# Optimization experiments

Measured on AMD Instinct MI355X. Metric: run time of the kernel, lower is better.

The kernel has to match this reference:

```python
import jax, jax.numpy as jnp
import numpy as np

WINDOW = 1
BETA = 0.01
EPS = 1e-6


def conv3x3(x, W, b):
    y = jax.lax.conv_general_dilated(x, W, (1, 1), 'SAME',
                                     dimension_numbers=('NCHW', 'OIHW', 'NCHW'))
    return y + b[None, :, None, None]


def grid_sample_bilinear(feat, gx, gy):
    # feat [n,C,H,W]; gx,gy [n,h,w] normalized to [-1,1]; align_corners=True, zeros padding
    n, C, H, W = feat.shape
    ix = (gx + 1.0) * 0.5 * (W - 1)
    iy = (gy + 1.0) * 0.5 * (H - 1)
    x0 = jnp.floor(ix)
    y0 = jnp.floor(iy)
    wx = ix - x0
    wy = iy - y0

    def corner(xc, yc, wgt):
        valid = (xc >= 0) & (xc <= W - 1) & (yc >= 0) & (yc <= H - 1)
        xi = jnp.clip(xc, 0, W - 1).astype(jnp.int32)
        yi = jnp.clip(yc, 0, H - 1).astype(jnp.int32)
        g = jax.vmap(lambda f, yy, xx: f[:, yy, xx])(feat, yi, xi)  # [n,C,h,w]
        return g * (wgt * valid)[:, None, :, :]

    return (corner(x0, y0, (1 - wx) * (1 - wy)) +
            corner(x0 + 1, y0, wx * (1 - wy)) +
            corner(x0, y0 + 1, (1 - wx) * wy) +
            corner(x0 + 1, y0 + 1, wx * wy))


def random_pooling(gt, rand, h, w):
    # adaptive_max_pool2d with exact-division output -> uniform block max pool
    n, c, H, W = gt.shape
    kh, kw = H // h, W // w
    rm = rand * (gt > 0.1)
    blocks = rm.reshape(n, c, h, kh, w, kw).transpose(0, 1, 2, 4, 3, 5)
    blocks = blocks.reshape(n, c, h, w, kh * kw)
    loc = jnp.argmax(blocks, axis=-1)
    bi, bj = loc // kw, loc % kw
    row = jnp.arange(h, dtype=jnp.int32)[:, None] * kh + bi
    col = jnp.arange(w, dtype=jnp.int32)[None, :] * kw + bj
    indices = row * W + col  # flat indices into H*W, [n,c,h,w]
    gtf = gt.reshape(n, c, H * W)
    rg = jnp.take_along_axis(gtf, indices.reshape(n, c, h * w), axis=-1)
    rg = rg.reshape(n, c, h, w)
    rg = jnp.where(rg < 0.1, 0.0, rg)
    return rg, indices


def log_grads(rg, window):
    # windowed log-gradients in 4 directions per offset distance
    n, c, h, w = rg.shape
    image = jnp.pad(rg, ((0, 0), (0, 0), (window, window), (window, window)))
    limg = jnp.log(image + EPS)
    mask = image > 0.1
    lc = limg[:, :, window:window + h, window:window + w]
    mc = mask[:, :, window:window + h, window:window + w]
    gs, ms = [], []
    for dd in range(1, window + 1):
        for ox, oy in ((0, dd), (dd, dd), (dd, 0), (dd, -dd)):
            sx, sy = window + ox, window + oy
            gs.append(lc - limg[:, :, sx:sx + h, sy:sy + w])
            ms.append(mc & mask[:, :, sx:sx + h, sy:sy + w])
    return jnp.concatenate(gs, 1), jnp.concatenate(ms, 1)


def single_loss(rand_i, x, d, gts, W_att, b_att, W_post, b_post):
    n, c, h, w = d.shape
    H, W = gts.shape[2], gts.shape[3]
    rg, indices = random_pooling(gts, rand_i, h, w)
    bias = W // w // 2 + (H // h // 2) * W
    indices = indices + bias
    ind_x = 2.0 * ((indices % W).astype(d.dtype) / W - 0.5)
    ind_y = 2.0 * ((indices // W).astype(d.dtype) / H - 0.5)
    feat = grid_sample_bilinear(x, ind_x[:, 0], ind_y[:, 0])
    att = jax.nn.sigmoid(conv3x3(feat, W_att, b_att))
    ds = conv3x3(att * d, W_post, b_post)
    grad_gt, grad_mk = log_grads(rg, WINDOW)
    a = jnp.abs(ds - grad_gt)
    sl1 = jnp.where(a < BETA, 0.5 * a * a / BETA, a - 0.5 * BETA)
    mk = grad_mk.astype(ds.dtype)
    return (sl1 * mk).sum() / mk.sum()


def setup_inputs() -> dict:
    key = jax.random.key(0)
    ks = jax.random.split(key, 8)
    n, H, W = 4, 480, 640
    h, w = 120, 160
    DC, FC, R = 32, 32, 20  # r = 5 * 4 * window
    return {
        'x': jax.random.normal(ks[0], (n, FC, H, W), dtype=jnp.float32),
        'd': jax.random.normal(ks[1], (n, DC, h, w), dtype=jnp.float32),
        'gts': jax.random.uniform(ks[2], (n, 1, H, W), dtype=jnp.float32),
        'rand': jax.random.uniform(ks[3], (R, n, 1, H, W), dtype=jnp.float32),
        'W_att': jax.random.normal(ks[4], (DC, FC, 3, 3), dtype=jnp.float32) * 0.05,
        'b_att': jnp.zeros((DC,), dtype=jnp.float32),
        'W_post': jax.random.normal(ks[5], (4 * WINDOW, DC, 3, 3), dtype=jnp.float32) * 0.05,
        'b_post': jnp.zeros((4 * WINDOW,), dtype=jnp.float32),
    }


def reference(x, d, gts, rand, W_att, b_att, W_post, b_post):
    def step(acc, r_i):
        return acc + single_loss(r_i, x, d, gts, W_att, b_att, W_post, b_post), None
    total, _ = jax.lax.scan(step, jnp.float32(0.0), rand)
    return total / rand.shape[0]
```

## Files before the change

### kernel.cpp

```cpp
#include <hip/hip_runtime.h>
#include <math.h>

#define NN 4
#define FC 32
#define DC 32
#define HH 480
#define WW 640
#define hh 120
#define ww 160
#define RR 20
#define TILE 14
#define ATT 16
#define FT 18
#define BIAS_IDX 1282
#define CP 16
#define LOGEPS -13.815511f
#define MTHR   -8.0f

#define WS_W1T 64
#define WS_W2T 9280
#define WS_WB1 10432
#define WS_WB2 15040
#define WS_RED 19648
#define WS_RG  20480
#define WS_IDX 1556480
#define WS_XB  3092480
#define XB_COUNT ((size_t)NN * HH * WW * 16)
#define WS_NEED_BYTES (((size_t)WS_XB + XB_COUNT) * 4)

#define XPACK_B0 1
#define XPACK_NB (HH * NN)
#define POOL_B0  (XPACK_B0 + XPACK_NB)
#define POOL_CB  (hh * ww / 256)
#define POOL_NB  (POOL_CB * NN * RR)
#define SETUP_NB (POOL_B0 + POOL_NB)

typedef __attribute__((ext_vector_type(8))) short short8;
typedef __attribute__((ext_vector_type(4))) float f32x4;
typedef __attribute__((ext_vector_type(2))) float f32x2;

__device__ __forceinline__ unsigned int bf16pack(float a, float b) {
    unsigned int ua = __float_as_uint(a);
    ua = (ua + 0x7fffu + ((ua >> 16) & 1u)) >> 16;
    unsigned int ub = __float_as_uint(b);
    ub = (ub + 0x7fffu + ((ub >> 16) & 1u)) >> 16;
    return ua | (ub << 16);
}
__device__ __forceinline__ unsigned short bf16r(float f) {
    unsigned int u = __float_as_uint(f);
    u = (u + 0x7fffu + ((u >> 16) & 1u)) >> 16;
    return (unsigned short)u;
}
__device__ __forceinline__ float bf16tof(unsigned short s) {
    return __uint_as_float(((unsigned int)s) << 16);
}

__global__ void setup_kernel(const float* __restrict__ x, const float* __restrict__ gts,
                             const float* __restrict__ rnd,
                             const float* __restrict__ W_att, const float* __restrict__ W_post,
                             float* __restrict__ ws) {
    const int b = blockIdx.x;
    const int tid = threadIdx.x;

    if (b == 0) {
        if (tid < 2*RR) ws[tid] = 0.f;
        for (int i = tid; i < RR*16*2; i += 256) ws[WS_RED + i] = 0.f;
        float* w1t = ws + WS_W1T;
        float* w2t = ws + WS_W2T;
        for (int i = tid; i < 32*32*9; i += 256) {
            int oc = i / (32*9); int rem = i % (32*9); int c = rem / 9; int tap = rem % 9;
            w1t[(tap*32 + c)*32 + oc] = W_att[i];
        }
        for (int i = tid; i < 4*32*9; i += 256) {
            int oc = i / (32*9); int rem = i % (32*9); int c = rem / 9; int tap = rem % 9;
            w2t[(tap*32 + c)*4 + oc] = W_post[i];
        }
        unsigned int* wb = (unsigned int*)(ws + WS_WB1);
        for (int i = tid; i < 9*2*64; i += 256) {
            int lane = i & 63; int th = i >> 6;
            int t = th >> 1, h2 = th & 1;
            int q = lane >> 4, col = lane & 15, oc = h2*16 + col;
            unsigned int vv[4];
            #pragma unroll
            for (int j = 0; j < 4; ++j) {
                int c0 = 8*q + 2*j;
                float f0 = W_att[(oc*32 + c0    )*9 + t];
                float f1 = W_att[(oc*32 + c0 + 1)*9 + t];
                vv[j] = bf16pack(f0, f1);
            }
            uint4 v4; v4.x = vv[0]; v4.y = vv[1]; v4.z = vv[2]; v4.w = vv[3];
            ((uint4*)wb)[i] = v4;
        }
        unsigned int* wb2 = (unsigned int*)(ws + WS_WB2);
        for (int i = tid; i < 9*2*64; i += 256) {
            int lane = i & 63; int th = i >> 6;
            int t = th >> 1, part = th & 1;
            int q = lane >> 4, oc = lane & 15;
            unsigned int vv[4];
            #pragma unroll
            for (int j = 0; j < 4; ++j) {
                int c0 = 8*q + 2*j;
                float f0 = (oc < 4) ? W_post[(oc*32 + c0    )*9 + t] : 0.f;
                float f1 = (oc < 4) ? W_post[(oc*32 + c0 + 1)*9 + t] : 0.f;
                if (part == 0) {
                    vv[j] = ((unsigned int)bf16r(f0)) | (((unsigned int)bf16r(f1)) << 16);
                } else {
                    float l0 = f0 - bf16tof(bf16r(f0));
                    float l1 = f1 - bf16tof(bf16r(f1));
                    vv[j] = ((unsigned int)bf16r(l0)) | (((unsigned int)bf16r(l1)) << 16);
                }
            }
            uint4 v4; v4.x = vv[0]; v4.y = vv[1]; v4.z = vv[2]; v4.w = vv[3];
            ((uint4*)wb2)[i] = v4;
        }
    } else if (b < POOL_B0) {
        const int bb = b - XPACK_B0;
        const int y = bb % HH;
        const int n = bb / HH;
        unsigned int* xb = (unsigned int*)(ws + WS_XB);
        for (int px = tid; px < WW; px += 256) {
            unsigned int* o = xb + ((size_t)(n*HH + y)*WW + px) * 16;
            uint4 v[4];
            #pragma unroll
            for (int k = 0; k < 4; ++k) {
                #pragma unroll
                for (int j = 0; j < 4; ++j) {
                    int cp = 4*k + j;
                    float f0 = x[((size_t)(n*FC + 2*cp    )*HH + y)*WW + px];
                    float f1 = x[((size_t)(n*FC + 2*cp + 1)*HH + y)*WW + px];
                    ((unsigned int*)&v[k])[j] = bf16pack(f0, f1);
                }
            }
            #pragma unroll
            for (int k = 0; k < 4; ++k) ((uint4*)o)[k] = v[k];
        }
    } else {
        const int bb = b - POOL_B0;
        const int r  = bb / (POOL_CB * NN);
        const int rem = bb % (POOL_CB * NN);
        const int n  = rem / POOL_CB;
        const int cb = rem % POOL_CB;
        const int cell = cb * 256 + tid;
        const int h = cell / ww, w = cell % ww;
        const float* gt_n = gts + (size_t)n * HH * WW;
        const float* rd_n = rnd + ((size_t)r * NN + n) * (size_t)(HH * WW);
        float best = -1.f, bg = 0.f; int bii = 0, bjj = 0;
        #pragma unroll
        for (int bi = 0; bi < 4; ++bi) {
            const float4 g4 = *(const float4*)(gt_n + (size_t)(h*4 + bi)*WW + w*4);
            const float4 r4 = *(const float4*)(rd_n + (size_t)(h*4 + bi)*WW + w*4);
            const float gv[4] = {g4.x, g4.y, g4.z, g4.w};
            const float rv[4] = {r4.x, r4.y, r4.z, r4.w};
            #pragma unroll
            for (int bj = 0; bj < 4; ++bj) {
                float rm = (gv[bj] > 0.1f) ? rv[bj] : 0.f;
                if (rm > best) { best = rm; bii = bi; bjj = bj; bg = gv[bj]; }
            }
        }
        int idx_b = (h*4 + bii) * WW + (w*4 + bjj) + BIAS_IDX;
        size_t o = ((size_t)(r*NN + n) * (hh*ww)) + cell;
        float g2 = (bg < 0.1f) ? 0.f : bg;
        ((float*)(ws + WS_RG))[o] = logf(g2 + 1e-6f);
        ((unsigned int*)(ws + WS_IDX))[o] = ((unsigned int)(idx_b / WW) << 16) | (unsigned int)(idx_b % WW);
    }
}

__launch_bounds__(256, 4)
__global__ void wvl_main(const unsigned int* __restrict__ xb, const float* __restrict__ d,
                         const float* __restrict__ b_att, const float* __restrict__ b_post,
                         float* __restrict__ ws) {
    __shared__ unsigned int s_feat[FT * FT * 16];
    __shared__ float s_plog[FT * FT];
    __shared__ float s_rn[4], s_rd[4];

    const float* lg_all  = (const float*)(ws + WS_RG);
    const unsigned int* pidx_all = (const unsigned int*)(ws + WS_IDX);

    const int tid = threadIdx.x;

    const int f   = blockIdx.x;
    const int xcd = f & 7;
    const int bb  = f >> 3;
    const int gi  = bb / 120;
    const int ii  = bb % 120;
    const int band = gi * 8 + xcd;
    const int n   = band / 18;
    const int rem = band % 18;
    const int ty  = rem >> 1;
    const int tx  = (rem & 1) * 6 + (ii % 6);
    const int r   = ii / 6;

    const int py0 = ty * TILE - 2;
    const int px0 = tx * TILE - 2;

    const size_t pbase = (size_t)(r*NN + n) * (hh*ww);

    for (int p = tid; p < FT * FT; p += 256) {
        int pi = p / FT, pj = p % FT;
        int gi2 = py0 + pi, gj = px0 + pj;
        float lval = LOGEPS;
        if (gi2 >= 0 && gi2 < hh && gj >= 0 && gj < ww)
            lval = lg_all[pbase + (size_t)gi2 * ww + gj];
        s_plog[p] = lval;
    }

    for (int p = tid; p < FT * FT; p += 256) {
        int pi = p / FT, pj = p % FT;
        int gi2 = py0 + pi, gj = px0 + pj;
        unsigned int* dst = &s_feat[p * 16];
        const int sw = (p >> 1) & 3;
        if (gi2 < 0 || gi2 >= hh || gj < 0 || gj >= ww) {
            uint4 z; z.x = z.y = z.z = z.w = 0u;
            #pragma unroll
            for (int k = 0; k < 4; ++k) ((uint4*)dst)[k] = z;
            continue;
        }
        unsigned int pk = pidx_all[pbase + (size_t)gi2 * ww + gj];
        int rr2 = (int)(pk >> 16);
        int cc  = (int)(pk & 0xffff);
        float gxf = 2.0f * ((float)cc  / (float)WW - 0.5f);
        float gyf = 2.0f * ((float)rr2 / (float)HH - 0.5f);
        float ix = (gxf + 1.0f) * 0.5f * (float)(WW - 1);
        float iy = (gyf + 1.0f) * 0.5f * (float)(HH - 1);
        float x0f = floorf(ix), y0f = floorf(iy);
        float wx = ix - x0f, wy = iy - y0f;
        int x0 = (int)x0f, y0 = (int)y0f;
        float vx0 = (x0f >= 0.f        && x0f <= (float)(WW-1)) ? 1.f : 0.f;
        float vx1 = (x0f + 1.f >= 0.f  && x0f + 1.f <= (float)(WW-1)) ? 1.f : 0.f;
        float vy0 = (y0f >= 0.f        && y0f <= (float)(HH-1)) ? 1.f : 0.f;
        float vy1 = (y0f + 1.f >= 0.f  && y0f + 1.f <= (float)(HH-1)) ? 1.f : 0.f;
        int xi0 = min(max(x0, 0), WW-1),  xi1 = min(max(x0+1, 0), WW-1);
        int yi0 = min(max(y0, 0), HH-1),  yi1 = min(max(y0+1, 0), HH-1);
        float w00 = (1.f-wx)*(1.f-wy) * (vx0*vy0);
        float w10 = wx*(1.f-wy)       * (vx1*vy0);
        float w01 = (1.f-wx)*wy       * (vx0*vy1);
        float w11 = wx*wy             * (vx1*vy1);
        const f32x2 vw00 = {w00, w00}, vw10 = {w10, w10}, vw01 = {w01, w01}, vw11 = {w11, w11};
        const uint4* q00 = (const uint4*)(xb + ((size_t)(n*HH + yi0)*WW + xi0) * 16);
        const uint4* q10 = (const uint4*)(xb + ((size_t)(n*HH + yi0)*WW + xi1) * 16);
        const uint4* q01 = (const uint4*)(xb + ((size_t)(n*HH + yi1)*WW + xi0) * 16);
        const uint4* q11 = (const uint4*)(xb + ((size_t)(n*HH + yi1)*WW + xi1) * 16);
        #pragma unroll
        for (int k = 0; k < 4; ++k) {
            uint4 A = q00[k], B = q10[k], C = q01[k], D = q11[k];
            uint4 o;
            #pragma unroll
            for (int j = 0; j < 4; ++j) {
                unsigned int ua = ((const unsigned int*)&A)[j];
                unsigned int ub = ((const unsigned int*)&B)[j];
                unsigned int uc = ((const unsigned int*)&C)[j];
                unsigned int ud = ((const unsigned int*)&D)[j];
                f32x2 va = {__uint_as_float(ua << 16), __uint_as_float(ua & 0xffff0000u)};
                f32x2 vb = {__uint_as_float(ub << 16), __uint_as_float(ub & 0xffff0000u)};
                f32x2 vc = {__uint_as_float(uc << 16), __uint_as_float(uc & 0xffff0000u)};
                f32x2 vd = {__uint_as_float(ud << 16), __uint_as_float(ud & 0xffff0000u)};
                f32x2 acc = vw00 * va;
                acc += vw10 * vb;
                acc += vw01 * vc;
                acc += vw11 * vd;
                ((unsigned int*)&o)[j] = bf16pack(acc.x, acc.y);
            }
            ((uint4*)dst)[k ^ sw] = o;
        }
    }
    __syncthreads();

    const int lane = tid & 63;
    const int wv   = tid >> 6;
    const int mcol = lane & 15;
    const int q    = lane >> 4;

    f32x4 acc1[4][2];
    {
        float bb0 = b_att[mcol];
        float bb1 = b_att[mcol + 16];
        #pragma unroll
        for (int rr = 0; rr < 4; ++rr) {
            acc1[rr][0] = (f32x4){bb0, bb0, bb0, bb0};
            acc1[rr][1] = (f32x4){bb1, bb1, bb1, bb1};
        }
    }
    {
        const uint4* wB = (const uint4*)(ws + WS_WB1);
        #pragma unroll
        for (int t = 0; t < 9; ++t) {
            union { uint4 u; short8 s; } b0u, b1u;
            b0u.u = wB[(t*2 + 0)*64 + lane];
            b1u.u = wB[(t*2 + 1)*64 + lane];
            const int dy = t / 3, dx = t % 3;
            #pragma unroll
            for (int rr = 0; rr < 4; ++rr) {
                int ay = wv*4 + rr;
                int pix = (ay + dy) * FT + dx + mcol;
                union { uint4 u; short8 s; } a;
                a.u = *(const uint4*)&s_feat[pix * 16 + (q ^ ((pix >> 1) & 3)) * 4];
                acc1[rr][0] = __builtin_amdgcn_mfma_f32_16x16x32_bf16(a.s, b0u.s, acc1[rr][0], 0, 0, 0);
                acc1[rr][1] = __builtin_amdgcn_mfma_f32_16x16x32_bf16(a.s, b1u.s, acc1[rr][1], 0, 0, 0);
            }
        }
    }
    __syncthreads();

    {
        unsigned short* attd16 = (unsigned short*)s_feat;
        #pragma unroll
        for (int rr = 0; rr < 4; ++rr) {
            int ay = wv*4 + rr;
            int gy = ty * TILE - 1 + ay;
            bool gyok = (gy >= 0 && gy < hh);
            #pragma unroll
            for (int h2 = 0; h2 < 2; ++h2) {
                int oc = mcol + 16*h2;
                const float* drow = d + ((size_t)(n*DC + oc) * hh + (gyok ? gy : 0)) * ww;
                #pragma unroll
                for (int reg = 0; reg < 4; ++reg) {
                    int ax = 4*q + reg;
                    int gx = tx * TILE - 1 + ax;
                    float av = __builtin_amdgcn_rcpf(1.f + __expf(-acc1[rr][h2][reg]));
                    float dv = (gyok && gx >= 0 && gx < ww) ? drow[gx] : 0.f;
                    int pix = ay * ATT + ax;
                    int dwi = pix * 16 + ((oc >> 3) ^ ((pix >> 1) & 3)) * 4 + ((oc >> 1) & 3);
                    attd16[dwi * 2 + (oc & 1)] = bf16r(av * dv);
                }
            }
        }
    }
    __syncthreads();

    float num_t = 0.f, den_t = 0.f;
    {
        const uint4* wB2 = (const uint4*)(ws + WS_WB2);
        const int qy0 = wv * 4;
        float bias2 = (mcol < 4) ? b_post[mcol] : 0.f;
        f32x4 acc2[4];
        #pragma unroll
        for (int rr = 0; rr < 4; ++rr) acc2[rr] = (f32x4){bias2, bias2, bias2, bias2};
        #pragma unroll
        for (int t = 0; t < 9; ++t) {
            union { uint4 u; short8 s; } bh, bl;
            bh.u = wB2[(t*2 + 0)*64 + lane];
            bl.u = wB2[(t*2 + 1)*64 + lane];
            const int dy = t / 3, dx = t % 3;
            #pragma unroll
            for (int rr = 0; rr < 4; ++rr) {
                if (qy0 + rr >= TILE) break;
                int pix = (qy0 + rr + dy) * ATT + (mcol + dx);
                union { uint4 u; short8 s; } a;
                a.u = *(const uint4*)&s_feat[pix * 16 + (q ^ ((pix >> 1) & 3)) * 4];
                acc2[rr] = __builtin_amdgcn_mfma_f32_16x16x32_bf16(a.s, bh.s, acc2[rr], 0, 0, 0);
                acc2[rr] = __builtin_amdgcn_mfma_f32_16x16x32_bf16(a.s, bl.s, acc2[rr], 0, 0, 0);
            }
        }
        const int o3 = mcol & 3;
        const int oy = (o3 == 0) ? 0 : 1;
        const int ox = (o3 == 3) ? -1 : ((o3 == 2) ? 0 : 1);
        #pragma unroll
        for (int rr = 0; rr < 4; ++rr) {
            if (qy0 + rr >= TILE) break;
            int qy = qy0 + rr;
            int gy2 = ty * TILE + qy;
            bool rowok = (gy2 < hh);
            #pragma unroll
            for (int reg = 0; reg < 4; ++reg) {
                int qx = 4*q + reg;
                int gx2 = tx * TILE + qx;
                float lc = s_plog[(qy + 2) * FT + (qx + 2)];
                float ln = s_plog[(qy + 2 + oy) * FT + (qx + 2 + ox)];
                bool m = rowok && (qx < TILE) && (gx2 < ww) && (mcol < 4)
                       && (lc > MTHR) && (ln > MTHR);
                float a2 = fabsf(acc2[rr][reg] - (lc - ln));
                float sl1 = (a2 < 0.01f) ? (50.f * a2 * a2) : (a2 - 0.005f);
                if (m) { num_t += sl1; den_t += 1.f; }
            }
        }
    }

    for (int off = 32; off > 0; off >>= 1) {
        num_t += __shfl_down(num_t, off);
        den_t += __shfl_down(den_t, off);
    }
    if (lane == 0) { s_rn[wv] = num_t; s_rd[wv] = den_t; }
    __syncthreads();
    if (tid == 0) {
        int slot = r * 16 + (bb & 15);
        atomicAdd(&ws[WS_RED + slot*2],     s_rn[0] + s_rn[1] + s_rn[2] + s_rn[3]);
        atomicAdd(&ws[WS_RED + slot*2 + 1], s_rd[0] + s_rd[1] + s_rd[2] + s_rd[3]);
    }
}

__launch_bounds__(256, 6)
__global__ void wvl_fallback(const float* __restrict__ x, const float* __restrict__ d,
                             const float* __restrict__ gts, const float* __restrict__ rnd,
                             const float* __restrict__ b_att, const float* __restrict__ b_post,
                             float* __restrict__ ws) {
    __shared__ unsigned int s_buf[CP * FT * FT];
    __shared__ float s_pgt[FT * FT];
    __shared__ int   s_pidx[FT * FT];
    __shared__ float s_rn[4], s_rd[4];

    const float* w1t = ws + WS_W1T;
    const float* w2t = ws + WS_W2T;

    const int tid = threadIdx.x;
    const int tilesx = (ww + TILE - 1) / TILE;
    const int tx = blockIdx.x % tilesx;
    const int ty = blockIdx.x / tilesx;
    const int n  = blockIdx.y;
    const int r  = blockIdx.z;
    const int py0 = ty * TILE - 2;
    const int px0 = tx * TILE - 2;

    const float* gt_n = gts + (size_t)n * HH * WW;
    const float* rd_n = rnd + ((size_t)r * NN + n) * (size_t)(HH * WW);
    for (int p = tid; p < FT * FT; p += 256) {
        int pi = p / FT, pj = p % FT;
        int gi = py0 + pi, gj = px0 + pj;
        float gval = 0.f; int idx = -1;
        if (gi >= 0 && gi < hh && gj >= 0 && gj < ww) {
            float best = -1.f; int bii = 0, bjj = 0; float bg = 0.f;
            #pragma unroll
            for (int bi = 0; bi < 4; ++bi) {
                const float* gr = gt_n + (size_t)(gi*4 + bi) * WW + gj*4;
                const float* rp = rd_n + (size_t)(gi*4 + bi) * WW + gj*4;
                #pragma unroll
                for (int bj = 0; bj < 4; ++bj) {
                    float g  = gr[bj];
                    float rv = rp[bj];
                    float rm = (g > 0.1f) ? rv : 0.f;
                    if (rm > best) { best = rm; bii = bi; bjj = bj; bg = g; }
                }
            }
            gval = bg;
            idx = (gi*4 + bii) * WW + (gj*4 + bjj) + BIAS_IDX;
        }
        s_pgt[p]  = gval;
        s_pidx[p] = idx;
    }
    __syncthreads();

    const float* x_n = x + (size_t)n * FC * HH * WW;
    for (int p = tid; p < FT * FT; p += 256) {
        int idx = s_pidx[p];
        if (idx < 0) {
            #pragma unroll
            for (int cp = 0; cp < CP; ++cp) s_buf[cp * (FT*FT) + p] = 0u;
            continue;
        }
        int cc = idx % WW;
        int rr2 = idx / WW;
        float gxf = 2.0f * ((float)cc  / (float)WW - 0.5f);
        float gyf = 2.0f * ((float)rr2 / (float)HH - 0.5f);
        float ix = (gxf + 1.0f) * 0.5f * (float)(WW - 1);
        float iy = (gyf + 1.0f) * 0.5f * (float)(HH - 1);
        float x0f = floorf(ix), y0f = floorf(iy);
        float wx = ix - x0f, wy = iy - y0f;
        int x0 = (int)x0f, y0 = (int)y0f;
        float vx0 = (x0f >= 0.f        && x0f <= (float)(WW-1)) ? 1.f : 0.f;
        float vx1 = (x0f + 1.f >= 0.f  && x0f + 1.f <= (float)(WW-1)) ? 1.f : 0.f;
        float vy0 = (y0f >= 0.f        && y0f <= (float)(HH-1)) ? 1.f : 0.f;
        float vy1 = (y0f + 1.f >= 0.f  && y0f + 1.f <= (float)(HH-1)) ? 1.f : 0.f;
        int xi0 = min(max(x0, 0), WW-1),  xi1 = min(max(x0+1, 0), WW-1);
        int yi0 = min(max(y0, 0), HH-1),  yi1 = min(max(y0+1, 0), HH-1);
        float w00 = (1.f-wx)*(1.f-wy) * (vx0*vy0);
        float w10 = wx*(1.f-wy)       * (vx1*vy0);
        float w01 = (1.f-wx)*wy       * (vx0*vy1);
        float w11 = wx*wy             * (vx1*vy1);
        const float* p00 = x_n + (size_t)yi0 * WW + xi0;
        const float* p10 = x_n + (size_t)yi0 * WW + xi1;
        const float* p01 = x_n + (size_t)yi1 * WW + xi0;
        const float* p11 = x_n + (size_t)yi1 * WW + xi1;
        #pragma unroll 4
        for (int cp = 0; cp < CP; ++cp) {
            int o0 = (2*cp)     * (HH * WW);
            int o1 = (2*cp + 1) * (HH * WW);
            float f0 = w00 * p00[o0] + w10 * p10[o0] + w01 * p01[o0] + w11 * p11[o0];
            float f1 = w00 * p00[o1] + w10 * p10[o1] + w01 * p01[o1] + w11 * p11[o1];
            s_buf[cp * (FT*FT) + p] = bf16pack(f0, f1);
        }
    }
    __syncthreads();

    const int ay = tid >> 4, ax = tid & 15;
    float acc[32];
    #pragma unroll
    for (int oc = 0; oc < 32; ++oc) acc[oc] = b_att[oc];
    for (int dy = 0; dy < 3; ++dy) {
        for (int dx = 0; dx < 3; ++dx) {
            const float* wt = w1t + (dy*3 + dx) * 1024;
            int base = (ay + dy) * FT + (ax + dx);
            for (int cp = 0; cp < CP; ++cp) {
                unsigned int u = s_buf[cp * (FT*FT) + base];
                float f0 = __uint_as_float(u << 16);
                float f1 = __uint_as_float(u & 0xffff0000u);
                const float* wp0 = wt + (2*cp) * 32;
                const float* wp1 = wp0 + 32;
                #pragma unroll
                for (int oc = 0; oc < 32; ++oc) acc[oc] = fmaf(f0, wp0[oc], acc[oc]);
                #pragma unroll
                for (int oc = 0; oc < 32; ++oc) acc[oc] = fmaf(f1, wp1[oc], acc[oc]);
            }
        }
    }
    __syncthreads();
    {
        int gy = ty * TILE - 1 + ay;
        int gx = tx * TILE - 1 + ax;
        bool inb = (gy >= 0 && gy < hh && gx >= 0 && gx < ww);
        const float* d_n = d + (size_t)n * DC * hh * ww;
        #pragma unroll
        for (int cp = 0; cp < CP; ++cp) {
            float a0 = 1.f / (1.f + __expf(-acc[2*cp]));
            float a1 = 1.f / (1.f + __expf(-acc[2*cp+1]));
            float v0 = 0.f, v1 = 0.f;
            if (inb) {
                v0 = a0 * d_n[(size_t)((2*cp)   * hh + gy) * ww + gx];
                v1 = a1 * d_n[(size_t)((2*cp+1) * hh + gy) * ww + gx];
            }
            s_buf[cp * (ATT*ATT) + tid] = bf16pack(v0, v1);
        }
    }
    __syncthreads();

    float num_t = 0.f, den_t = 0.f;
    if (tid < TILE * TILE) {
        int qy = tid / TILE, qx = tid % TILE;
        int gy2 = ty * TILE + qy, gx2 = tx * TILE + qx;
        if (gy2 < hh && gx2 < ww) {
            float acc2[4];
            #pragma unroll
            for (int k = 0; k < 4; ++k) acc2[k] = b_post[k];
            for (int dy = 0; dy < 3; ++dy) {
                for (int dx = 0; dx < 3; ++dx) {
                    const float* wt = w2t + (dy*3 + dx) * 128;
                    int base = (qy + dy) * ATT + (qx + dx);
                    for (int cp = 0; cp < CP; ++cp) {
                        unsigned int u = s_buf[cp * (ATT*ATT) + base];
                        float f0 = __uint_as_float(u << 16);
                        float f1 = __uint_as_float(u & 0xffff0000u);
                        const float* wp0 = wt + (2*cp) * 4;
                        const float* wp1 = wp0 + 4;
                        #pragma unroll
                        for (int k2 = 0; k2 < 4; ++k2) acc2[k2] = fmaf(f0, wp0[k2], acc2[k2]);
                        #pragma unroll
                        for (int k2 = 0; k2 < 4; ++k2) acc2[k2] = fmaf(f1, wp1[k2], acc2[k2]);
                    }
                }
            }
            int pc = (qy + 2) * FT + (qx + 2);
            float rgc = s_pgt[pc]; rgc = (rgc < 0.1f) ? 0.f : rgc;
            float lc = logf(rgc + 1e-6f);
            bool  mc = rgc > 0.1f;
            const int oys[4] = {0, 1, 1, 1};
            const int oxs[4] = {1, 1, 0, -1};
            #pragma unroll
            for (int k = 0; k < 4; ++k) {
                int pnb = (qy + 2 + oys[k]) * FT + (qx + 2 + oxs[k]);
                float rgn = s_pgt[pnb]; rgn = (rgn < 0.1f) ? 0.f : rgn;
                float ln = logf(rgn + 1e-6f);
                bool m = mc && (rgn > 0.1f);
                float gg = lc - ln;
                float a2 = fabsf(acc2[k] - gg);
                float sl1 = (a2 < 0.01f) ? (0.5f * a2 * a2 / 0.01f) : (a2 - 0.005f);
                if (m) { num_t += sl1; den_t += 1.f; }
            }
        }
    }
    for (int off = 32; off > 0; off >>= 1) {
        num_t += __shfl_down(num_t, off);
        den_t += __shfl_down(den_t, off);
    }
    int wid = tid >> 6, lane = tid & 63;
    if (lane == 0) { s_rn[wid] = num_t; s_rd[wid] = den_t; }
    __syncthreads();
    if (tid == 0) {
        int slot = r * 16 + (blockIdx.x & 15);
        atomicAdd(&ws[WS_RED + slot*2],     s_rn[0] + s_rn[1] + s_rn[2] + s_rn[3]);
        atomicAdd(&ws[WS_RED + slot*2 + 1], s_rd[0] + s_rd[1] + s_rd[2] + s_rd[3]);
    }
}

__global__ void finish_kernel(const float* __restrict__ ws, float* __restrict__ out) {
    __shared__ float sn[RR], sd[RR];
    const int tid = threadIdx.x;
    if (tid < RR) { sn[tid] = 0.f; sd[tid] = 0.f; }
    __syncthreads();
    if (tid < RR * 16) {
        int r2 = tid >> 4;
        atomicAdd(&sn[r2], ws[WS_RED + tid*2]);
        atomicAdd(&sd[r2], ws[WS_RED + tid*2 + 1]);
    }
    __syncthreads();
    if (tid == 0) {
        float s = 0.f;
        for (int r2 = 0; r2 < RR; ++r2) s += sn[r2] / sd[r2];
        out[0] = s / (float)RR;
    }
}

extern "C" void kernel_launch(void* const* d_in, const int* in_sizes, int n_in,
                              void* d_out, int out_size, void* d_ws, size_t ws_size,
                              hipStream_t stream) {
    const float* x      = (const float*)d_in[0];
    const float* d      = (const float*)d_in[1];
    const float* gts    = (const float*)d_in[2];
    const float* rnd    = (const float*)d_in[3];
    const float* W_att  = (const float*)d_in[4];
    const float* b_att  = (const float*)d_in[5];
    const float* W_post = (const float*)d_in[6];
    const float* b_post = (const float*)d_in[7];
    float* out = (float*)d_out;
    float* ws  = (float*)d_ws;

    const int tilesx = (ww + TILE - 1) / TILE;
    const int tilesy = (hh + TILE - 1) / TILE;

    if (ws_size >= WS_NEED_BYTES) {
        hipLaunchKernelGGL(setup_kernel, dim3(SETUP_NB), dim3(256), 0, stream,
                           x, gts, rnd, W_att, W_post, ws);
        unsigned int* xb = (unsigned int*)(ws + WS_XB);
        hipLaunchKernelGGL(wvl_main, dim3(tilesx * tilesy * NN * RR), dim3(256), 0, stream,
                           xb, d, b_att, b_post, ws);
    } else {
        hipLaunchKernelGGL(setup_kernel, dim3(1), dim3(256), 0, stream,
                           x, gts, rnd, W_att, W_post, ws);
        dim3 grid2(tilesx * tilesy, NN, RR);
        hipLaunchKernelGGL(wvl_fallback, grid2, dim3(256), 0, stream,
                           x, d, gts, rnd, b_att, b_post, ws);
    }

    hipLaunchKernelGGL(finish_kernel, dim3(1), dim3(512), 0, stream, ws, out);
}
```

Before: 581.0 us.

## Pre-pack d channel-last and transpose MFMA operands for vectorized epilogues

Adds a setup stage that repacks the depth feature tensor d into a per-pixel channel-contiguous layout in the workspace. Swaps the A/B operands of both MFMA convolutions so each lane holds four consecutive output channels of one pixel. The attention-times-d epilogue can then use two float4 loads and two packed 8-byte LDS stores, replacing many scattered scalar global loads and 2-byte shared stores. The loss epilogue now reads one centre log value per row. This costs an extra workspace buffer and an extra pass over d in setup, which is repeated work across the 20 random draws only once.

```diff
diff --git a/kernel.cpp b/kernel.cpp
--- a/kernel.cpp
+++ b/kernel.cpp
@@ -26,14 +26,18 @@
 #define WS_IDX 1556480
 #define WS_XB  3092480
 #define XB_COUNT ((size_t)NN * HH * WW * 16)
-#define WS_NEED_BYTES (((size_t)WS_XB + XB_COUNT) * 4)
+#define WS_DPK (WS_XB + 19660800)
+#define DPK_COUNT ((size_t)NN * hh * ww * 32)
+#define WS_NEED_BYTES (((size_t)WS_DPK + DPK_COUNT) * 4)
 
 #define XPACK_B0 1
 #define XPACK_NB (HH * NN)
 #define POOL_B0  (XPACK_B0 + XPACK_NB)
 #define POOL_CB  (hh * ww / 256)
 #define POOL_NB  (POOL_CB * NN * RR)
-#define SETUP_NB (POOL_B0 + POOL_NB)
+#define DPK_B0   (POOL_B0 + POOL_NB)
+#define DPK_NB   (NN * hh)
+#define SETUP_NB (DPK_B0 + DPK_NB)
 
 typedef __attribute__((ext_vector_type(8))) short short8;
 typedef __attribute__((ext_vector_type(4))) float f32x4;
@@ -55,8 +59,8 @@
     return __uint_as_float(((unsigned int)s) << 16);
 }
 
-__global__ void setup_kernel(const float* __restrict__ x, const float* __restrict__ gts,
-                             const float* __restrict__ rnd,
+__global__ void setup_kernel(const float* __restrict__ x, const float* __restrict__ d,
+                             const float* __restrict__ gts, const float* __restrict__ rnd,
                              const float* __restrict__ W_att, const float* __restrict__ W_post,
                              float* __restrict__ ws) {
     const int b = blockIdx.x;
@@ -134,7 +138,7 @@
             #pragma unroll
             for (int k = 0; k < 4; ++k) ((uint4*)o)[k] = v[k];
         }
-    } else {
+    } else if (b < DPK_B0) {
         const int bb = b - POOL_B0;
         const int r  = bb / (POOL_CB * NN);
         const int rem = bb % (POOL_CB * NN);
@@ -162,11 +166,27 @@
         float g2 = (bg < 0.1f) ? 0.f : bg;
         ((float*)(ws + WS_RG))[o] = logf(g2 + 1e-6f);
         ((unsigned int*)(ws + WS_IDX))[o] = ((unsigned int)(idx_b / WW) << 16) | (unsigned int)(idx_b % WW);
+    } else {
+        const int bb = b - DPK_B0;
+        const int n = bb / hh;
+        const int y = bb % hh;
+        float* dpk = ws + WS_DPK;
+        if (tid < ww) {
+            int px = tid;
+            float v[32];
+            #pragma unroll
+            for (int c = 0; c < 32; ++c)
+                v[c] = d[((size_t)(n*DC + c) * hh + y) * ww + px];
+            float* o = dpk + ((size_t)(n*hh + y)*ww + px) * 32;
+            #pragma unroll
+            for (int k = 0; k < 8; ++k)
+                ((float4*)o)[k] = *(const float4*)&v[4*k];
+        }
     }
 }
 
 __launch_bounds__(256, 4)
-__global__ void wvl_main(const unsigned int* __restrict__ xb, const float* __restrict__ d,
+__global__ void wvl_main(const unsigned int* __restrict__ xb,
                          const float* __restrict__ b_att, const float* __restrict__ b_post,
                          float* __restrict__ ws) {
     __shared__ unsigned int s_feat[FT * FT * 16];
@@ -272,12 +292,12 @@
 
     f32x4 acc1[4][2];
     {
-        float bb0 = b_att[mcol];
-        float bb1 = b_att[mcol + 16];
+        const f32x4 bv0 = ((const f32x4*)b_att)[q];
+        const f32x4 bv1 = ((const f32x4*)b_att)[4 + q];
         #pragma unroll
         for (int rr = 0; rr < 4; ++rr) {
-            acc1[rr][0] = (f32x4){bb0, bb0, bb0, bb0};
-            acc1[rr][1] = (f32x4){bb1, bb1, bb1, bb1};
+            acc1[rr][0] = bv0;
+            acc1[rr][1] = bv1;
         }
     }
     {
@@ -294,35 +314,42 @@
                 int pix = (ay + dy) * FT + dx + mcol;
                 union { uint4 u; short8 s; } a;
                 a.u = *(const uint4*)&s_feat[pix * 16 + (q ^ ((pix >> 1) & 3)) * 4];
-                acc1[rr][0] = __builtin_amdgcn_mfma_f32_16x16x32_bf16(a.s, b0u.s, acc1[rr][0], 0, 0, 0);
-                acc1[rr][1] = __builtin_amdgcn_mfma_f32_16x16x32_bf16(a.s, b1u.s, acc1[rr][1], 0, 0, 0);
+                acc1[rr][0] = __builtin_amdgcn_mfma_f32_16x16x32_bf16(b0u.s, a.s, acc1[rr][0], 0, 0, 0);
+                acc1[rr][1] = __builtin_amdgcn_mfma_f32_16x16x32_bf16(b1u.s, a.s, acc1[rr][1], 0, 0, 0);
             }
         }
     }
     __syncthreads();
 
     {
-        unsigned short* attd16 = (unsigned short*)s_feat;
+        const float* dpk = ws + WS_DPK;
+        const int gx = tx * TILE - 1 + mcol;
+        const bool gxok = (gx >= 0 && gx < ww);
+        const int gxs = min(max(gx, 0), ww - 1);
         #pragma unroll
         for (int rr = 0; rr < 4; ++rr) {
             int ay = wv*4 + rr;
             int gy = ty * TILE - 1 + ay;
-            bool gyok = (gy >= 0 && gy < hh);
-            #pragma unroll
-            for (int h2 = 0; h2 < 2; ++h2) {
-                int oc = mcol + 16*h2;
-                const float* drow = d + ((size_t)(n*DC + oc) * hh + (gyok ? gy : 0)) * ww;
-                #pragma unroll
-                for (int reg = 0; reg < 4; ++reg) {
-                    int ax = 4*q + reg;
-                    int gx = tx * TILE - 1 + ax;
-                    float av = __builtin_amdgcn_rcpf(1.f + __expf(-acc1[rr][h2][reg]));
-                    float dv = (gyok && gx >= 0 && gx < ww) ? drow[gx] : 0.f;
-                    int pix = ay * ATT + ax;
-                    int dwi = pix * 16 + ((oc >> 3) ^ ((pix >> 1) & 3)) * 4 + ((oc >> 1) & 3);
-                    attd16[dwi * 2 + (oc & 1)] = bf16r(av * dv);
-                }
-            }
+            bool ok = gxok && (gy >= 0 && gy < hh);
+            int gys = min(max(gy, 0), hh - 1);
+            const float* dp = dpk + ((size_t)((n*hh + gys)*ww + gxs)) * 32;
+            f32x4 d0 = *(const f32x4*)(dp + 4*q);
+            f32x4 d1 = *(const f32x4*)(dp + 16 + 4*q);
+            if (!ok) { d0 = (f32x4){0,0,0,0}; d1 = (f32x4){0,0,0,0}; }
+            float v0[4], v1[4];
+            #pragma unroll
+            for (int reg = 0; reg < 4; ++reg) {
+                v0[reg] = __builtin_amdgcn_rcpf(1.f + __expf(-acc1[rr][0][reg])) * d0[reg];
+                v1[reg] = __builtin_amdgcn_rcpf(1.f + __expf(-acc1[rr][1][reg])) * d1[reg];
+            }
+            int pix = ay * ATT + mcol;
+            int sw2 = (pix >> 1) & 3;
+            int dwA = pix * 16 + (((q >> 1)    ) ^ sw2) * 4 + ((2*q) & 3);
+            int dwB = pix * 16 + (((q >> 1) + 2) ^ sw2) * 4 + ((2*q) & 3);
+            uint2 pa; pa.x = bf16pack(v0[0], v0[1]); pa.y = bf16pack(v0[2], v0[3]);
+            uint2 pb; pb.x = bf16pack(v1[0], v1[1]); pb.y = bf16pack(v1[2], v1[3]);
+            *(uint2*)&s_feat[dwA] = pa;
+            *(uint2*)&s_feat[dwB] = pb;
         }
     }
     __syncthreads();
@@ -331,10 +358,10 @@
     {
         const uint4* wB2 = (const uint4*)(ws + WS_WB2);
         const int qy0 = wv * 4;
-        float bias2 = (mcol < 4) ? b_post[mcol] : 0.f;
+        const f32x4 bias2v = *((const f32x4*)b_post);
         f32x4 acc2[4];
         #pragma unroll
-        for (int rr = 0; rr < 4; ++rr) acc2[rr] = (f32x4){bias2, bias2, bias2, bias2};
+        for (int rr = 0; rr < 4; ++rr) acc2[rr] = bias2v;
         #pragma unroll
         for (int t = 0; t < 9; ++t) {
             union { uint4 u; short8 s; } bh, bl;
@@ -347,27 +374,23 @@
                 int pix = (qy0 + rr + dy) * ATT + (mcol + dx);
                 union { uint4 u; short8 s; } a;
                 a.u = *(const uint4*)&s_feat[pix * 16 + (q ^ ((pix >> 1) & 3)) * 4];
-                acc2[rr] = __builtin_amdgcn_mfma_f32_16x16x32_bf16(a.s, bh.s, acc2[rr], 0, 0, 0);
-                acc2[rr] = __builtin_amdgcn_mfma_f32_16x16x32_bf16(a.s, bl.s, acc2[rr], 0, 0, 0);
-            }
-        }
-        const int o3 = mcol & 3;
-        const int oy = (o3 == 0) ? 0 : 1;
-        const int ox = (o3 == 3) ? -1 : ((o3 == 2) ? 0 : 1);
+                acc2[rr] = __builtin_amdgcn_mfma_f32_16x16x32_bf16(bh.s, a.s, acc2[rr], 0, 0, 0);
+                acc2[rr] = __builtin_amdgcn_mfma_f32_16x16x32_bf16(bl.s, a.s, acc2[rr], 0, 0, 0);
+            }
+        }
+        const bool colok = (q == 0) && (mcol < TILE) && (tx * TILE + mcol < ww);
         #pragma unroll
         for (int rr = 0; rr < 4; ++rr) {
             if (qy0 + rr >= TILE) break;
             int qy = qy0 + rr;
-            int gy2 = ty * TILE + qy;
-            bool rowok = (gy2 < hh);
+            bool rowok = (ty * TILE + qy < hh);
+            float lc = s_plog[(qy + 2) * FT + (mcol + 2)];
+            const int oys[4] = {0, 1, 1, 1};
+            const int oxs[4] = {1, 1, 0, -1};
             #pragma unroll
             for (int reg = 0; reg < 4; ++reg) {
-                int qx = 4*q + reg;
-                int gx2 = tx * TILE + qx;
-                float lc = s_plog[(qy + 2) * FT + (qx + 2)];
-                float ln = s_plog[(qy + 2 + oy) * FT + (qx + 2 + ox)];
-                bool m = rowok && (qx < TILE) && (gx2 < ww) && (mcol < 4)
-                       && (lc > MTHR) && (ln > MTHR);
+                float ln = s_plog[(qy + 2 + oys[reg]) * FT + (mcol + 2 + oxs[reg])];
+                bool m = colok && rowok && (lc > MTHR) && (ln > MTHR);
                 float a2 = fabsf(acc2[rr][reg] - (lc - ln));
                 float sl1 = (a2 < 0.01f) ? (50.f * a2 * a2) : (a2 - 0.005f);
                 if (m) { num_t += sl1; den_t += 1.f; }
@@ -616,13 +639,13 @@
 
     if (ws_size >= WS_NEED_BYTES) {
         hipLaunchKernelGGL(setup_kernel, dim3(SETUP_NB), dim3(256), 0, stream,
-                           x, gts, rnd, W_att, W_post, ws);
+                           x, d, gts, rnd, W_att, W_post, ws);
         unsigned int* xb = (unsigned int*)(ws + WS_XB);
         hipLaunchKernelGGL(wvl_main, dim3(tilesx * tilesy * NN * RR), dim3(256), 0, stream,
-                           xb, d, b_att, b_post, ws);
+                           xb, b_att, b_post, ws);
     } else {
         hipLaunchKernelGGL(setup_kernel, dim3(1), dim3(256), 0, stream,
-                           x, gts, rnd, W_att, W_post, ws);
+                           x, d, gts, rnd, W_att, W_post, ws);
         dim3 grid2(tilesx * tilesy, NN, RR);
         hipLaunchKernelGGL(wvl_fallback, grid2, dim3(256), 0, stream,
                            x, d, gts, rnd, b_att, b_post, ws);
```

Result: faster. 498.5 us (-14.2%).
